# Kernel tuning notes

Measured on AMD Instinct MI355X. Metric: run time of the kernel, lower is better.

Reference implementation:

```python
import jax, jax.numpy as jnp
import numpy as np

# kernel_size=3, dilate=1 -> kernel_sample[3]=[0,1,2,3,4] selects these 5 (dy,dx) offsets
OFFSETS = [(-1, -1), (-1, 0), (-1, 1), (0, -1), (0, 0)]
EPS = 1e-12  # F.normalize default eps


def setup_inputs() -> dict:
    key = jax.random.key(0)
    x = jax.random.normal(key, (16, 192, 64, 64), dtype=jnp.float32)
    return {"x": x}


def reference(x):
    B, C, H, W = x.shape
    # ReplicationPad2d(kernel_size//2 = 1) == edge padding
    xp = jnp.pad(x, ((0, 0), (0, 0), (1, 1), (1, 1)), mode="edge")
    # centers are all interior pixels of the padded map == original pixels
    center = x.reshape(B, C, H * W).transpose(0, 2, 1)  # (B, K, C), K = H*W
    cofe = []
    for dy, dx in OFFSETS:
        side = xp[:, :, 1 + dy:1 + dy + H, 1 + dx:1 + dx + W]
        side = side.reshape(B, C, H * W).transpose(0, 2, 1)  # (B, K, C)
        # sum over K of outer products center_k (x) side_k -> (B, C, C)
        co = jnp.einsum('bkc,bkd->bcd', center, side).reshape(B, C * C)
        cofe.append(co)
    cofe = jnp.stack(cofe, axis=1)  # (B, 5, C*C)
    norm = jnp.linalg.norm(cofe, axis=-1, keepdims=True)
    return cofe / jnp.maximum(norm, EPS)
```

## Files before the change

kernel.cpp:

```cpp
#include <hip/hip_runtime.h>
#include <stdint.h>

#define C_CH 192
#define HW   4096
#define NB   16
#define NO   5

typedef __attribute__((ext_vector_type(8)))  short short8;
typedef __attribute__((ext_vector_type(16))) float floatx16;

__device__ __forceinline__ unsigned short f2bf(float f) {
    unsigned int u = __float_as_uint(f);
    unsigned int r = (u + 0x7fffu + ((u >> 16) & 1u)) >> 16;
    return (unsigned short)r;
}

__device__ __forceinline__ uint4 s8u4(short8 f) { return *(uint4*)&f; }

__device__ __forceinline__ short8 shift_m(short8 f, unsigned short ex) {
    uint4 v = *(uint4*)&f; uint4 w;
    w.x = (unsigned)ex   | (v.x << 16);
    w.y = (v.x >> 16)    | (v.y << 16);
    w.z = (v.y >> 16)    | (v.z << 16);
    w.w = (v.z >> 16)    | (v.w << 16);
    return *(short8*)&w;
}
__device__ __forceinline__ short8 shift_p(short8 f, unsigned short ex) {
    uint4 v = *(uint4*)&f; uint4 w;
    w.x = (v.x >> 16) | (v.y << 16);
    w.y = (v.y >> 16) | (v.z << 16);
    w.z = (v.z >> 16) | (v.w << 16);
    w.w = (v.w >> 16) | ((unsigned)ex << 16);
    return *(short8*)&w;
}

#define MAKE_SHIFT(Uarr, S, Um, Up)                                              \
    do {                                                                         \
        uint4 _u0 = s8u4(Uarr[(S) > 0 ? (S) - 1 : 0]);                           \
        uint4 _u1 = s8u4(Uarr[S]);                                               \
        uint4 _u2 = s8u4(Uarr[(S) < 3 ? (S) + 1 : 3]);                           \
        unsigned _sm = lo ? _u0.w : _u1.w;                                       \
        unsigned _sp = lo ? _u1.x : _u2.x;                                       \
        unsigned _rm = (unsigned)__shfl_xor((int)_sm, 32, 64);                   \
        unsigned _rp = (unsigned)__shfl_xor((int)_sp, 32, 64);                   \
        unsigned short _exm = (unsigned short)(_rm >> 16);                       \
        if ((S) == 0) _exm = lo ? _exm : (unsigned short)(_u1.x & 0xffffu);      \
        unsigned short _exp = (unsigned short)(_rp & 0xffffu);                   \
        if ((S) == 3) _exp = lo ? (unsigned short)(_u1.w >> 16) : _exp;          \
        Um = shift_m(Uarr[S], _exm);                                             \
        Up = shift_p(Uarr[S], _exp);                                             \
    } while (0)

__global__ __launch_bounds__(256) void convert_kernel(const float* __restrict__ x,
                                                      unsigned short* __restrict__ xb,
                                                      float* __restrict__ norms) {
    if (blockIdx.x == 0 && threadIdx.x < NB * NO) norms[threadIdx.x] = 0.0f;
    int t   = blockIdx.x * 256 + threadIdx.x;
    int grp = t >> 14;
    int idx = t & 16383;
    int qhi = idx >> 8;
    int cp  = (idx >> 3) & 31;
    int qlo = idx & 7;
    int q   = qhi * 8 + qlo;
    int b   = grp / 6;
    int cb  = grp - b * 6;
    int ch  = cb * 32 + cp;
    const float4* p = (const float4*)(x + (size_t)(b * C_CH + ch) * HW + q * 8);
    float4 v0 = p[0], v1 = p[1];
    ushort4 o0, o1;
    o0.x = f2bf(v0.x); o0.y = f2bf(v0.y); o0.z = f2bf(v0.z); o0.w = f2bf(v0.w);
    o1.x = f2bf(v1.x); o1.y = f2bf(v1.y); o1.z = f2bf(v1.z); o1.w = f2bf(v1.w);
    ushort4* dst = (ushort4*)xb + ((size_t)grp * 16384 + q * 32 + cp) * 2;
    dst[0] = o0; dst[1] = o1;
}

__global__ __launch_bounds__(512) void cofe_gemm(const unsigned short* __restrict__ xb,
                                                 float* __restrict__ out,
                                                 float* __restrict__ norms) {
    constexpr int RW = 8;
    int blk  = blockIdx.x;
    int work = (blk & 7) * 72 + (blk >> 3);
    int b = work / 36;
    int t = work % 36;
    int cbA = t / 6, cbB = t % 6;
    int c0 = cbA * 32, d0 = cbB * 32;

    int wv   = threadIdx.x >> 6;
    int lane = threadIdx.x & 63;
    int lr   = lane & 31;
    int lo   = lane >> 5;
    int laneoff = lo * 32 + lr;

    const short8* A8 = (const short8*)xb + (size_t)(b * 6 + cbA) * 16384;
    const short8* B8 = (const short8*)xb + (size_t)(b * 6 + cbB) * 16384;

    floatx16 acc[5];
    #pragma unroll
    for (int o = 0; o < 5; ++o)
        #pragma unroll
        for (int e = 0; e < 16; ++e)
            acc[o][e] = 0.0f;

    int h0 = wv * RW;

    short8 U[2][4];
    short8 A[3][4];

    #pragma unroll
    for (int s = 0; s < 4; ++s) {
        U[0][s] = B8[(8 * h0 + 2 * s) * 32 + laneoff];
        A[0][s] = A8[(8 * h0 + 2 * s) * 32 + laneoff];
        A[1][s] = A8[(8 * (h0 + 1) + 2 * s) * 32 + laneoff];
    }

    if (h0 == 0) {
        #pragma unroll
        for (int s = 0; s < 4; ++s) {
            short8 Um, Up;
            MAKE_SHIFT(U[0], s, Um, Up);
            acc[0] = __builtin_amdgcn_mfma_f32_32x32x16_bf16(A[0][s], Um,      acc[0], 0, 0, 0);
            acc[1] = __builtin_amdgcn_mfma_f32_32x32x16_bf16(A[0][s], U[0][s], acc[1], 0, 0, 0);
            acc[2] = __builtin_amdgcn_mfma_f32_32x32x16_bf16(A[0][s], Up,      acc[2], 0, 0, 0);
        }
    }

    #pragma unroll
    for (int r = 0; r < RW; ++r) {
        int g  = h0 + r;
        const int cu = r & 1, nx = (r + 1) & 1;
        const int ia = r % 3, ib = (r + 1) % 3, ic = (r + 2) % 3;
        int ga = (g + 2 < 64) ? g + 2 : 63;
        int gu = (g + 1 < 64) ? g + 1 : 63;
        #pragma unroll
        for (int s = 0; s < 4; ++s) {
            A[ic][s] = A8[(8 * ga + 2 * s) * 32 + laneoff];
            U[nx][s] = B8[(8 * gu + 2 * s) * 32 + laneoff];

            short8 Um, Up;
            MAKE_SHIFT(U[cu], s, Um, Up);

            acc[4] = __builtin_amdgcn_mfma_f32_32x32x16_bf16(A[ia][s], U[cu][s], acc[4], 0, 0, 0);
            acc[3] = __builtin_amdgcn_mfma_f32_32x32x16_bf16(A[ia][s], Um,       acc[3], 0, 0, 0);
            if (r + 1 < RW || g < 63) {
                acc[1] = __builtin_amdgcn_mfma_f32_32x32x16_bf16(A[ib][s], U[cu][s], acc[1], 0, 0, 0);
                acc[0] = __builtin_amdgcn_mfma_f32_32x32x16_bf16(A[ib][s], Um,       acc[0], 0, 0, 0);
                acc[2] = __builtin_amdgcn_mfma_f32_32x32x16_bf16(A[ib][s], Up,       acc[2], 0, 0, 0);
            }
        }
    }

    __shared__ float red[8192];
    __shared__ float wsum[4];
    float4* red4 = (float4*)red;
    size_t obase = (size_t)b * NO * (C_CH * C_CH);
    int tt = threadIdx.x;

    for (int o = 0; o < 5; ++o) {
        __syncthreads();
        #pragma unroll
        for (int reg = 0; reg < 16; ++reg) {
            int row = (reg & 3) + 8 * (reg >> 2) + 4 * lo;
            red[wv * 1024 + row * 32 + lr] = acc[o][reg];
        }
        __syncthreads();
        if (tt < 256) {
            float4 s = red4[tt];
            #pragma unroll
            for (int seg = 1; seg < 8; ++seg) {
                float4 v = red4[seg * 256 + tt];
                s.x += v.x; s.y += v.y; s.z += v.z; s.w += v.w;
            }
            int row = tt >> 3;
            int col = (tt & 7) * 4;
            float* op = out + obase + (size_t)o * (C_CH * C_CH)
                      + (size_t)(c0 + row) * C_CH + d0 + col;
            *(float4*)op = s;

            float ss = s.x * s.x + s.y * s.y + s.z * s.z + s.w * s.w;
            #pragma unroll
            for (int off = 32; off; off >>= 1) ss += __shfl_down(ss, off, 64);
            if (lane == 0) wsum[tt >> 6] = ss;
        }
        __syncthreads();
        if (tt == 0) atomicAdd(&norms[b * NO + o], wsum[0] + wsum[1] + wsum[2] + wsum[3]);
    }
}

__global__ __launch_bounds__(256) void scale_kernel(float* __restrict__ out,
                                                    const float* __restrict__ norms) {
    int g  = blockIdx.x * 256 + threadIdx.x;
    int bo = blockIdx.x / 36;
    float s = norms[bo];
    float inv = 1.0f / fmaxf(sqrtf(s), 1e-12f);
    float4 v = ((const float4*)out)[g];
    v.x *= inv; v.y *= inv; v.z *= inv; v.w *= inv;
    ((float4*)out)[g] = v;
}

extern "C" void kernel_launch(void* const* d_in, const int* in_sizes, int n_in,
                              void* d_out, int out_size, void* d_ws, size_t ws_size,
                              hipStream_t stream) {
    const float* x = (const float*)d_in[0];
    float* out = (float*)d_out;
    float* norms = (float*)d_ws;
    unsigned short* xb = (unsigned short*)((char*)d_ws + 512);

    convert_kernel<<<6144, 256, 0, stream>>>(x, xb, norms);
    cofe_gemm<<<576, 512, 0, stream>>>(xb, out, norms);
    scale_kernel<<<2880, 256, 0, stream>>>(out, norms);
}
```

Baseline: 130.1 us.

## Split cofe GEMM into two passes to cut accumulator registers and raise occupancy

The main GEMM loop now runs twice. The first pass accumulates only the two same-row offsets (3, 4) and reduces and stores them. The second pass reloads the inputs and accumulates the three upper-row offsets (0, 1, 2). This cuts live accumulators from five 16-float tiles to at most three and the A buffers from three sets to one, and launch bounds now request 4 waves per EU, aiming for higher occupancy. In exchange, each block reads its input tiles from global memory twice and runs the loop overhead twice.

```diff
diff --git a/kernel.cpp b/kernel.cpp
--- a/kernel.cpp
+++ b/kernel.cpp
@@ -49,6 +49,17 @@
         if ((S) == 3) _exp = lo ? (unsigned short)(_u1.w >> 16) : _exp;          \
         Um = shift_m(Uarr[S], _exm);                                             \
         Up = shift_p(Uarr[S], _exp);                                             \
+    } while (0)
+
+#define MAKE_SHIFT_M(Uarr, S, Um)                                                \
+    do {                                                                         \
+        uint4 _u0 = s8u4(Uarr[(S) > 0 ? (S) - 1 : 0]);                           \
+        uint4 _u1 = s8u4(Uarr[S]);                                               \
+        unsigned _sm = lo ? _u0.w : _u1.w;                                       \
+        unsigned _rm = (unsigned)__shfl_xor((int)_sm, 32, 64);                   \
+        unsigned short _exm = (unsigned short)(_rm >> 16);                       \
+        if ((S) == 0) _exm = lo ? _exm : (unsigned short)(_u1.x & 0xffffu);      \
+        Um = shift_m(Uarr[S], _exm);                                             \
     } while (0)
 
 __global__ __launch_bounds__(256) void convert_kernel(const float* __restrict__ x,
@@ -74,10 +85,9 @@
     dst[0] = o0; dst[1] = o1;
 }
 
-__global__ __launch_bounds__(512) void cofe_gemm(const unsigned short* __restrict__ xb,
-                                                 float* __restrict__ out,
-                                                 float* __restrict__ norms) {
-    constexpr int RW = 8;
+__global__ __launch_bounds__(512, 4) void cofe_gemm(const unsigned short* __restrict__ xb,
+                                                    float* __restrict__ out,
+                                                    float* __restrict__ norms) {
     int blk  = blockIdx.x;
     int work = (blk & 7) * 72 + (blk >> 3);
     int b = work / 36;
@@ -94,60 +104,7 @@
     const short8* A8 = (const short8*)xb + (size_t)(b * 6 + cbA) * 16384;
     const short8* B8 = (const short8*)xb + (size_t)(b * 6 + cbB) * 16384;
 
-    floatx16 acc[5];
-    #pragma unroll
-    for (int o = 0; o < 5; ++o)
-        #pragma unroll
-        for (int e = 0; e < 16; ++e)
-            acc[o][e] = 0.0f;
-
-    int h0 = wv * RW;
-
-    short8 U[2][4];
-    short8 A[3][4];
-
-    #pragma unroll
-    for (int s = 0; s < 4; ++s) {
-        U[0][s] = B8[(8 * h0 + 2 * s) * 32 + laneoff];
-        A[0][s] = A8[(8 * h0 + 2 * s) * 32 + laneoff];
-        A[1][s] = A8[(8 * (h0 + 1) + 2 * s) * 32 + laneoff];
-    }
-
-    if (h0 == 0) {
-        #pragma unroll
-        for (int s = 0; s < 4; ++s) {
-            short8 Um, Up;
-            MAKE_SHIFT(U[0], s, Um, Up);
-            acc[0] = __builtin_amdgcn_mfma_f32_32x32x16_bf16(A[0][s], Um,      acc[0], 0, 0, 0);
-            acc[1] = __builtin_amdgcn_mfma_f32_32x32x16_bf16(A[0][s], U[0][s], acc[1], 0, 0, 0);
-            acc[2] = __builtin_amdgcn_mfma_f32_32x32x16_bf16(A[0][s], Up,      acc[2], 0, 0, 0);
-        }
-    }
-
-    #pragma unroll
-    for (int r = 0; r < RW; ++r) {
-        int g  = h0 + r;
-        const int cu = r & 1, nx = (r + 1) & 1;
-        const int ia = r % 3, ib = (r + 1) % 3, ic = (r + 2) % 3;
-        int ga = (g + 2 < 64) ? g + 2 : 63;
-        int gu = (g + 1 < 64) ? g + 1 : 63;
-        #pragma unroll
-        for (int s = 0; s < 4; ++s) {
-            A[ic][s] = A8[(8 * ga + 2 * s) * 32 + laneoff];
-            U[nx][s] = B8[(8 * gu + 2 * s) * 32 + laneoff];
-
-            short8 Um, Up;
-            MAKE_SHIFT(U[cu], s, Um, Up);
-
-            acc[4] = __builtin_amdgcn_mfma_f32_32x32x16_bf16(A[ia][s], U[cu][s], acc[4], 0, 0, 0);
-            acc[3] = __builtin_amdgcn_mfma_f32_32x32x16_bf16(A[ia][s], Um,       acc[3], 0, 0, 0);
-            if (r + 1 < RW || g < 63) {
-                acc[1] = __builtin_amdgcn_mfma_f32_32x32x16_bf16(A[ib][s], U[cu][s], acc[1], 0, 0, 0);
-                acc[0] = __builtin_amdgcn_mfma_f32_32x32x16_bf16(A[ib][s], Um,       acc[0], 0, 0, 0);
-                acc[2] = __builtin_amdgcn_mfma_f32_32x32x16_bf16(A[ib][s], Up,       acc[2], 0, 0, 0);
-            }
-        }
-    }
+    int h0 = wv * 8;
 
     __shared__ float red[8192];
     __shared__ float wsum[4];
@@ -155,35 +112,119 @@
     size_t obase = (size_t)b * NO * (C_CH * C_CH);
     int tt = threadIdx.x;
 
-    for (int o = 0; o < 5; ++o) {
-        __syncthreads();
-        #pragma unroll
-        for (int reg = 0; reg < 16; ++reg) {
-            int row = (reg & 3) + 8 * (reg >> 2) + 4 * lo;
-            red[wv * 1024 + row * 32 + lr] = acc[o][reg];
-        }
-        __syncthreads();
-        if (tt < 256) {
-            float4 s = red4[tt];
+#define REDUCE_STORE(ACC, O)                                                     \
+    do {                                                                         \
+        __syncthreads();                                                         \
+        _Pragma("unroll")                                                        \
+        for (int reg = 0; reg < 16; ++reg) {                                     \
+            int row_ = (reg & 3) + 8 * (reg >> 2) + 4 * lo;      \
+            red[wv * 1024 + row_ * 32 + lr] = ACC[reg];                          \
+        }                                                                        \
+        __syncthreads();                                                         \
+        if (tt < 256) {                                                          \
+            float4 sv = red4[tt];                                                \
+            _Pragma("unroll")                                                    \
+            for (int seg = 1; seg < 8; ++seg) {                                  \
+                float4 v = red4[seg * 256 + tt];                                 \
+                sv.x += v.x; sv.y += v.y; sv.z += v.z; sv.w += v.w;              \
+            }                                                                    \
+            int row_ = tt >> 3;                                                  \
+            int col_ = (tt & 7) * 4;                                             \
+            float* op = out + obase + (size_t)(O) * (C_CH * C_CH)                \
+                      + (size_t)(c0 + row_) * C_CH + d0 + col_;                  \
+            *(float4*)op = sv;                                                   \
+            float ss = sv.x * sv.x + sv.y * sv.y + sv.z * sv.z + sv.w * sv.w;    \
+            _Pragma("unroll")                                                    \
+            for (int off = 32; off; off >>= 1) ss += __shfl_down(ss, off, 64);   \
+            if (lane == 0) wsum[tt >> 6] = ss;                                   \
+        }                                                                        \
+        __syncthreads();                                                         \
+        if (tt == 0) atomicAdd(&norms[b * NO + (O)],                             \
+                               wsum[0] + wsum[1] + wsum[2] + wsum[3]);           \
+    } while (0)
+
+    short8 A[4];
+    short8 U[2][4];
+
+    {
+        floatx16 acc3, acc4;
+        #pragma unroll
+        for (int e = 0; e < 16; ++e) { acc3[e] = 0.0f; acc4[e] = 0.0f; }
+
+        #pragma unroll
+        for (int s = 0; s < 4; ++s) {
+            A[s]    = A8[(8 * h0 + 2 * s) * 32 + laneoff];
+            U[0][s] = B8[(8 * h0 + 2 * s) * 32 + laneoff];
+        }
+
+        #pragma unroll
+        for (int r = 0; r < 8; ++r) {
+            int g = h0 + r;
+            const int cu = r & 1, nx = (r + 1) & 1;
+            int gn = (g + 1 < 64) ? g + 1 : 63;
             #pragma unroll
-            for (int seg = 1; seg < 8; ++seg) {
-                float4 v = red4[seg * 256 + tt];
-                s.x += v.x; s.y += v.y; s.z += v.z; s.w += v.w;
+            for (int s = 0; s < 4; ++s) {
+                short8 Um;
+                MAKE_SHIFT_M(U[cu], s, Um);
+                acc4 = __builtin_amdgcn_mfma_f32_32x32x16_bf16(A[s], U[cu][s], acc4, 0, 0, 0);
+                acc3 = __builtin_amdgcn_mfma_f32_32x32x16_bf16(A[s], Um,       acc3, 0, 0, 0);
+                A[s]     = A8[(8 * gn + 2 * s) * 32 + laneoff];
+                U[nx][s] = B8[(8 * gn + 2 * s) * 32 + laneoff];
             }
-            int row = tt >> 3;
-            int col = (tt & 7) * 4;
-            float* op = out + obase + (size_t)o * (C_CH * C_CH)
-                      + (size_t)(c0 + row) * C_CH + d0 + col;
-            *(float4*)op = s;
-
-            float ss = s.x * s.x + s.y * s.y + s.z * s.z + s.w * s.w;
+        }
+
+        REDUCE_STORE(acc3, 3);
+        REDUCE_STORE(acc4, 4);
+    }
+
+    {
+        floatx16 acc0, acc1, acc2;
+        #pragma unroll
+        for (int e = 0; e < 16; ++e) { acc0[e] = 0.0f; acc1[e] = 0.0f; acc2[e] = 0.0f; }
+
+        #pragma unroll
+        for (int s = 0; s < 4; ++s) {
+            A[s]    = A8[(8 * (h0 + 1) + 2 * s) * 32 + laneoff];
+            U[0][s] = B8[(8 * h0 + 2 * s) * 32 + laneoff];
+        }
+
+        if (h0 == 0) {
             #pragma unroll
-            for (int off = 32; off; off >>= 1) ss += __shfl_down(ss, off, 64);
-            if (lane == 0) wsum[tt >> 6] = ss;
-        }
-        __syncthreads();
-        if (tt == 0) atomicAdd(&norms[b * NO + o], wsum[0] + wsum[1] + wsum[2] + wsum[3]);
+            for (int s = 0; s < 4; ++s) {
+                short8 A0 = A8[(2 * s) * 32 + laneoff];
+                short8 Um, Up;
+                MAKE_SHIFT(U[0], s, Um, Up);
+                acc0 = __builtin_amdgcn_mfma_f32_32x32x16_bf16(A0, Um,      acc0, 0, 0, 0);
+                acc1 = __builtin_amdgcn_mfma_f32_32x32x16_bf16(A0, U[0][s], acc1, 0, 0, 0);
+                acc2 = __builtin_amdgcn_mfma_f32_32x32x16_bf16(A0, Up,      acc2, 0, 0, 0);
+            }
+        }
+
+        #pragma unroll
+        for (int r = 0; r < 8; ++r) {
+            int g = h0 + r;
+            const int cu = r & 1, nx = (r + 1) & 1;
+            int gn  = (g + 1 < 64) ? g + 1 : 63;
+            int gnA = (g + 2 < 64) ? g + 2 : 63;
+            #pragma unroll
+            for (int s = 0; s < 4; ++s) {
+                if (r < 7 || g < 63) {
+                    short8 Um, Up;
+                    MAKE_SHIFT(U[cu], s, Um, Up);
+                    acc1 = __builtin_amdgcn_mfma_f32_32x32x16_bf16(A[s], U[cu][s], acc1, 0, 0, 0);
+                    acc0 = __builtin_amdgcn_mfma_f32_32x32x16_bf16(A[s], Um,       acc0, 0, 0, 0);
+                    acc2 = __builtin_amdgcn_mfma_f32_32x32x16_bf16(A[s], Up,       acc2, 0, 0, 0);
+                }
+                A[s]     = A8[(8 * gnA + 2 * s) * 32 + laneoff];
+                U[nx][s] = B8[(8 * gn  + 2 * s) * 32 + laneoff];
+            }
+        }
+
+        REDUCE_STORE(acc0, 0);
+        REDUCE_STORE(acc1, 1);
+        REDUCE_STORE(acc2, 2);
     }
+#undef REDUCE_STORE
 }
 
 __global__ __launch_bounds__(256) void scale_kernel(float* __restrict__ out,
```

New measurement: 139.0 us. 1.07x slower.

## Compute two A channel blocks per workgroup with fewer waves and longer row strips

Applied to the files above, without the earlier changes.

Each workgroup now computes a 64x32 output tile (two 32-row A blocks) sharing one B/shift stream, so each loaded B fragment and its shifted variants feed twice as many MFMAs. Waves per block drop from 8 to 4, each covering 16 rows instead of 8, and the grid halves to 288 blocks, which reduces the cross-wave shared-memory reduction work. The cost is doubled accumulator registers (10 floatx16), forcing one block per CU, fewer blocks than CUs, and lower latency hiding.

```diff
diff --git a/kernel.cpp b/kernel.cpp
--- a/kernel.cpp
+++ b/kernel.cpp
@@ -74,16 +74,16 @@
     dst[0] = o0; dst[1] = o1;
 }
 
-__global__ __launch_bounds__(512) void cofe_gemm(const unsigned short* __restrict__ xb,
-                                                 float* __restrict__ out,
-                                                 float* __restrict__ norms) {
-    constexpr int RW = 8;
+__global__ __launch_bounds__(256, 1) void cofe_gemm(const unsigned short* __restrict__ xb,
+                                                    float* __restrict__ out,
+                                                    float* __restrict__ norms) {
+    constexpr int RW = 16;
     int blk  = blockIdx.x;
-    int work = (blk & 7) * 72 + (blk >> 3);
-    int b = work / 36;
-    int t = work % 36;
-    int cbA = t / 6, cbB = t % 6;
-    int c0 = cbA * 32, d0 = cbB * 32;
+    int work = (blk & 7) * 36 + (blk >> 3);
+    int b = work / 18;
+    int t = work % 18;
+    int cbA2 = t / 6, cbB = t % 6;
+    int d0 = cbB * 32;
 
     int wv   = threadIdx.x >> 6;
     int lane = threadIdx.x & 63;
@@ -91,26 +91,29 @@
     int lo   = lane >> 5;
     int laneoff = lo * 32 + lr;
 
-    const short8* A8 = (const short8*)xb + (size_t)(b * 6 + cbA) * 16384;
-    const short8* B8 = (const short8*)xb + (size_t)(b * 6 + cbB) * 16384;
-
-    floatx16 acc[5];
+    const short8* A8a = (const short8*)xb + (size_t)(b * 6 + cbA2 * 2) * 16384;
+    const short8* A8b = A8a + 16384;
+    const short8* B8  = (const short8*)xb + (size_t)(b * 6 + cbB) * 16384;
+
+    floatx16 acc_a[5], acc_b[5];
     #pragma unroll
     for (int o = 0; o < 5; ++o)
         #pragma unroll
-        for (int e = 0; e < 16; ++e)
-            acc[o][e] = 0.0f;
+        for (int e = 0; e < 16; ++e) { acc_a[o][e] = 0.0f; acc_b[o][e] = 0.0f; }
 
     int h0 = wv * RW;
 
     short8 U[2][4];
-    short8 A[3][4];
+    short8 Aa[3][4];
+    short8 Ab[3][4];
 
     #pragma unroll
     for (int s = 0; s < 4; ++s) {
-        U[0][s] = B8[(8 * h0 + 2 * s) * 32 + laneoff];
-        A[0][s] = A8[(8 * h0 + 2 * s) * 32 + laneoff];
-        A[1][s] = A8[(8 * (h0 + 1) + 2 * s) * 32 + laneoff];
+        U[0][s]  = B8 [(8 * h0 + 2 * s) * 32 + laneoff];
+        Aa[0][s] = A8a[(8 * h0 + 2 * s) * 32 + laneoff];
+        Ab[0][s] = A8b[(8 * h0 + 2 * s) * 32 + laneoff];
+        Aa[1][s] = A8a[(8 * (h0 + 1) + 2 * s) * 32 + laneoff];
+        Ab[1][s] = A8b[(8 * (h0 + 1) + 2 * s) * 32 + laneoff];
     }
 
     if (h0 == 0) {
@@ -118,9 +121,12 @@
         for (int s = 0; s < 4; ++s) {
             short8 Um, Up;
             MAKE_SHIFT(U[0], s, Um, Up);
-            acc[0] = __builtin_amdgcn_mfma_f32_32x32x16_bf16(A[0][s], Um,      acc[0], 0, 0, 0);
-            acc[1] = __builtin_amdgcn_mfma_f32_32x32x16_bf16(A[0][s], U[0][s], acc[1], 0, 0, 0);
-            acc[2] = __builtin_amdgcn_mfma_f32_32x32x16_bf16(A[0][s], Up,      acc[2], 0, 0, 0);
+            acc_a[0] = __builtin_amdgcn_mfma_f32_32x32x16_bf16(Aa[0][s], Um,      acc_a[0], 0, 0, 0);
+            acc_a[1] = __builtin_amdgcn_mfma_f32_32x32x16_bf16(Aa[0][s], U[0][s], acc_a[1], 0, 0, 0);
+            acc_a[2] = __builtin_amdgcn_mfma_f32_32x32x16_bf16(Aa[0][s], Up,      acc_a[2], 0, 0, 0);
+            acc_b[0] = __builtin_amdgcn_mfma_f32_32x32x16_bf16(Ab[0][s], Um,      acc_b[0], 0, 0, 0);
+            acc_b[1] = __builtin_amdgcn_mfma_f32_32x32x16_bf16(Ab[0][s], U[0][s], acc_b[1], 0, 0, 0);
+            acc_b[2] = __builtin_amdgcn_mfma_f32_32x32x16_bf16(Ab[0][s], Up,      acc_b[2], 0, 0, 0);
         }
     }
 
@@ -133,57 +139,66 @@
         int gu = (g + 1 < 64) ? g + 1 : 63;
         #pragma unroll
         for (int s = 0; s < 4; ++s) {
-            A[ic][s] = A8[(8 * ga + 2 * s) * 32 + laneoff];
-            U[nx][s] = B8[(8 * gu + 2 * s) * 32 + laneoff];
+            Aa[ic][s] = A8a[(8 * ga + 2 * s) * 32 + laneoff];
+            Ab[ic][s] = A8b[(8 * ga + 2 * s) * 32 + laneoff];
+            U[nx][s]  = B8 [(8 * gu + 2 * s) * 32 + laneoff];
 
             short8 Um, Up;
             MAKE_SHIFT(U[cu], s, Um, Up);
 
-            acc[4] = __builtin_amdgcn_mfma_f32_32x32x16_bf16(A[ia][s], U[cu][s], acc[4], 0, 0, 0);
-            acc[3] = __builtin_amdgcn_mfma_f32_32x32x16_bf16(A[ia][s], Um,       acc[3], 0, 0, 0);
+            acc_a[4] = __builtin_amdgcn_mfma_f32_32x32x16_bf16(Aa[ia][s], U[cu][s], acc_a[4], 0, 0, 0);
+            acc_b[4] = __builtin_amdgcn_mfma_f32_32x32x16_bf16(Ab[ia][s], U[cu][s], acc_b[4], 0, 0, 0);
+            acc_a[3] = __builtin_amdgcn_mfma_f32_32x32x16_bf16(Aa[ia][s], Um,       acc_a[3], 0, 0, 0);
+            acc_b[3] = __builtin_amdgcn_mfma_f32_32x32x16_bf16(Ab[ia][s], Um,       acc_b[3], 0, 0, 0);
             if (r + 1 < RW || g < 63) {
-                acc[1] = __builtin_amdgcn_mfma_f32_32x32x16_bf16(A[ib][s], U[cu][s], acc[1], 0, 0, 0);
-                acc[0] = __builtin_amdgcn_mfma_f32_32x32x16_bf16(A[ib][s], Um,       acc[0], 0, 0, 0);
-                acc[2] = __builtin_amdgcn_mfma_f32_32x32x16_bf16(A[ib][s], Up,       acc[2], 0, 0, 0);
+                acc_a[1] = __builtin_amdgcn_mfma_f32_32x32x16_bf16(Aa[ib][s], U[cu][s], acc_a[1], 0, 0, 0);
+                acc_b[1] = __builtin_amdgcn_mfma_f32_32x32x16_bf16(Ab[ib][s], U[cu][s], acc_b[1], 0, 0, 0);
+                acc_a[0] = __builtin_amdgcn_mfma_f32_32x32x16_bf16(Aa[ib][s], Um,       acc_a[0], 0, 0, 0);
+                acc_b[0] = __builtin_amdgcn_mfma_f32_32x32x16_bf16(Ab[ib][s], Um,       acc_b[0], 0, 0, 0);
+                acc_a[2] = __builtin_amdgcn_mfma_f32_32x32x16_bf16(Aa[ib][s], Up,       acc_a[2], 0, 0, 0);
+                acc_b[2] = __builtin_amdgcn_mfma_f32_32x32x16_bf16(Ab[ib][s], Up,       acc_b[2], 0, 0, 0);
             }
         }
     }
 
-    __shared__ float red[8192];
+    __shared__ float red[4096];
     __shared__ float wsum[4];
     float4* red4 = (float4*)red;
     size_t obase = (size_t)b * NO * (C_CH * C_CH);
     int tt = threadIdx.x;
 
-    for (int o = 0; o < 5; ++o) {
-        __syncthreads();
-        #pragma unroll
-        for (int reg = 0; reg < 16; ++reg) {
-            int row = (reg & 3) + 8 * (reg >> 2) + 4 * lo;
-            red[wv * 1024 + row * 32 + lr] = acc[o][reg];
-        }
-        __syncthreads();
-        if (tt < 256) {
-            float4 s = red4[tt];
-            #pragma unroll
-            for (int seg = 1; seg < 8; ++seg) {
-                float4 v = red4[seg * 256 + tt];
-                s.x += v.x; s.y += v.y; s.z += v.z; s.w += v.w;
-            }
-            int row = tt >> 3;
-            int col = (tt & 7) * 4;
-            float* op = out + obase + (size_t)o * (C_CH * C_CH)
-                      + (size_t)(c0 + row) * C_CH + d0 + col;
-            *(float4*)op = s;
-
-            float ss = s.x * s.x + s.y * s.y + s.z * s.z + s.w * s.w;
-            #pragma unroll
-            for (int off = 32; off; off >>= 1) ss += __shfl_down(ss, off, 64);
-            if (lane == 0) wsum[tt >> 6] = ss;
-        }
-        __syncthreads();
-        if (tt == 0) atomicAdd(&norms[b * NO + o], wsum[0] + wsum[1] + wsum[2] + wsum[3]);
-    }
+#define EPILOGUE(ACC, C0)                                                        \
+    for (int o = 0; o < 5; ++o) {                                                \
+        __syncthreads();                                                         \
+        _Pragma("unroll")                                                        \
+        for (int reg = 0; reg < 16; ++reg) {                                     \
+            int row_ = (reg & 3) + 8 * (reg >> 2) + 4 * lo;      \
+            red[wv * 1024 + row_ * 32 + lr] = ACC[o][reg];                       \
+        }                                                                        \
+        __syncthreads();                                                         \
+        float4 sv = red4[tt];                                                    \
+        _Pragma("unroll")                                                        \
+        for (int seg = 1; seg < 4; ++seg) {                                      \
+            float4 v = red4[seg * 256 + tt];                                     \
+            sv.x += v.x; sv.y += v.y; sv.z += v.z; sv.w += v.w;                  \
+        }                                                                        \
+        int row_ = tt >> 3;                                                      \
+        int col_ = (tt & 7) * 4;                                                 \
+        float* op = out + obase + (size_t)o * (C_CH * C_CH)                      \
+                  + (size_t)((C0) + row_) * C_CH + d0 + col_;                    \
+        *(float4*)op = sv;                                                       \
+        float ss = sv.x * sv.x + sv.y * sv.y + sv.z * sv.z + sv.w * sv.w;        \
+        _Pragma("unroll")                                                        \
+        for (int off = 32; off; off >>= 1) ss += __shfl_down(ss, off, 64);       \
+        if (lane == 0) wsum[wv] = ss;                                            \
+        __syncthreads();                                                         \
+        if (tt == 0) atomicAdd(&norms[b * NO + o],                               \
+                               wsum[0] + wsum[1] + wsum[2] + wsum[3]);           \
+    }
+
+    EPILOGUE(acc_a, cbA2 * 64)
+    EPILOGUE(acc_b, cbA2 * 64 + 32)
+#undef EPILOGUE
 }
 
 __global__ __launch_bounds__(256) void scale_kernel(float* __restrict__ out,
@@ -206,6 +221,6 @@
     unsigned short* xb = (unsigned short*)((char*)d_ws + 512);
 
     convert_kernel<<<6144, 256, 0, stream>>>(x, xb, norms);
-    cofe_gemm<<<576, 512, 0, stream>>>(xb, out, norms);
+    cofe_gemm<<<288, 256, 0, stream>>>(xb, out, norms);
     scale_kernel<<<2880, 256, 0, stream>>>(out, norms);
 }
```

After: 151.1 us. 1.16x slower.

## Precompute shifted bf16 panels in convert kernel and halve GEMM block width

Applied to the files above, without the earlier changes.

The convert kernel now writes three bf16 panels: the center and copies shifted one pixel left and right, with edge replication handled through wave shuffles. The GEMM kernel then loads these shifted operands directly instead of building them with per-iteration shuffles and bit shifts. The GEMM also drops from 8 to 4 waves per block, each covering 16 rows instead of 8, so the cross-wave LDS reduction is shorter, and launch bounds request 2 blocks per CU. The cost is three times the workspace writes and triple B-operand global traffic, plus more register pressure and less row parallelism per block.

```diff
diff --git a/kernel.cpp b/kernel.cpp
--- a/kernel.cpp
+++ b/kernel.cpp
@@ -5,6 +5,7 @@
 #define HW   4096
 #define NB   16
 #define NO   5
+#define PANEL 25165824
 
 typedef __attribute__((ext_vector_type(8)))  short short8;
 typedef __attribute__((ext_vector_type(16))) float floatx16;
@@ -15,44 +16,10 @@
     return (unsigned short)r;
 }
 
-__device__ __forceinline__ uint4 s8u4(short8 f) { return *(uint4*)&f; }
-
-__device__ __forceinline__ short8 shift_m(short8 f, unsigned short ex) {
-    uint4 v = *(uint4*)&f; uint4 w;
-    w.x = (unsigned)ex   | (v.x << 16);
-    w.y = (v.x >> 16)    | (v.y << 16);
-    w.z = (v.y >> 16)    | (v.z << 16);
-    w.w = (v.z >> 16)    | (v.w << 16);
-    return *(short8*)&w;
-}
-__device__ __forceinline__ short8 shift_p(short8 f, unsigned short ex) {
-    uint4 v = *(uint4*)&f; uint4 w;
-    w.x = (v.x >> 16) | (v.y << 16);
-    w.y = (v.y >> 16) | (v.z << 16);
-    w.z = (v.z >> 16) | (v.w << 16);
-    w.w = (v.w >> 16) | ((unsigned)ex << 16);
-    return *(short8*)&w;
-}
-
-#define MAKE_SHIFT(Uarr, S, Um, Up)                                              \
-    do {                                                                         \
-        uint4 _u0 = s8u4(Uarr[(S) > 0 ? (S) - 1 : 0]);                           \
-        uint4 _u1 = s8u4(Uarr[S]);                                               \
-        uint4 _u2 = s8u4(Uarr[(S) < 3 ? (S) + 1 : 3]);                           \
-        unsigned _sm = lo ? _u0.w : _u1.w;                                       \
-        unsigned _sp = lo ? _u1.x : _u2.x;                                       \
-        unsigned _rm = (unsigned)__shfl_xor((int)_sm, 32, 64);                   \
-        unsigned _rp = (unsigned)__shfl_xor((int)_sp, 32, 64);                   \
-        unsigned short _exm = (unsigned short)(_rm >> 16);                       \
-        if ((S) == 0) _exm = lo ? _exm : (unsigned short)(_u1.x & 0xffffu);      \
-        unsigned short _exp = (unsigned short)(_rp & 0xffffu);                   \
-        if ((S) == 3) _exp = lo ? (unsigned short)(_u1.w >> 16) : _exp;          \
-        Um = shift_m(Uarr[S], _exm);                                             \
-        Up = shift_p(Uarr[S], _exp);                                             \
-    } while (0)
-
 __global__ __launch_bounds__(256) void convert_kernel(const float* __restrict__ x,
                                                       unsigned short* __restrict__ xb,
+                                                      unsigned short* __restrict__ xbm,
+                                                      unsigned short* __restrict__ xbp,
                                                       float* __restrict__ norms) {
     if (blockIdx.x == 0 && threadIdx.x < NB * NO) norms[threadIdx.x] = 0.0f;
     int t   = blockIdx.x * 256 + threadIdx.x;
@@ -67,17 +34,41 @@
     int ch  = cb * 32 + cp;
     const float4* p = (const float4*)(x + (size_t)(b * C_CH + ch) * HW + q * 8);
     float4 v0 = p[0], v1 = p[1];
-    ushort4 o0, o1;
-    o0.x = f2bf(v0.x); o0.y = f2bf(v0.y); o0.z = f2bf(v0.z); o0.w = f2bf(v0.w);
-    o1.x = f2bf(v1.x); o1.y = f2bf(v1.y); o1.z = f2bf(v1.z); o1.w = f2bf(v1.w);
-    ushort4* dst = (ushort4*)xb + ((size_t)grp * 16384 + q * 32 + cp) * 2;
-    dst[0] = o0; dst[1] = o1;
-}
-
-__global__ __launch_bounds__(512) void cofe_gemm(const unsigned short* __restrict__ xb,
-                                                 float* __restrict__ out,
-                                                 float* __restrict__ norms) {
-    constexpr int RW = 8;
+    unsigned u0 = (unsigned)f2bf(v0.x) | ((unsigned)f2bf(v0.y) << 16);
+    unsigned u1 = (unsigned)f2bf(v0.z) | ((unsigned)f2bf(v0.w) << 16);
+    unsigned u2 = (unsigned)f2bf(v1.x) | ((unsigned)f2bf(v1.y) << 16);
+    unsigned u3 = (unsigned)f2bf(v1.z) | ((unsigned)f2bf(v1.w) << 16);
+
+    unsigned prev_u3 = (unsigned)__shfl_up((int)u3, 1, 64);
+    unsigned next_u0 = (unsigned)__shfl_down((int)u0, 1, 64);
+    unsigned short exm = (qlo == 0) ? (unsigned short)(u0 & 0xffffu)
+                                    : (unsigned short)(prev_u3 >> 16);
+    unsigned short exp_ = (qlo == 7) ? (unsigned short)(u3 >> 16)
+                                     : (unsigned short)(next_u0 & 0xffffu);
+
+    uint4 cen = {u0, u1, u2, u3};
+    uint4 um, up;
+    um.x = (unsigned)exm | (u0 << 16);
+    um.y = (u0 >> 16)    | (u1 << 16);
+    um.z = (u1 >> 16)    | (u2 << 16);
+    um.w = (u2 >> 16)    | (u3 << 16);
+    up.x = (u0 >> 16)    | (u1 << 16);
+    up.y = (u1 >> 16)    | (u2 << 16);
+    up.z = (u2 >> 16)    | (u3 << 16);
+    up.w = (u3 >> 16)    | ((unsigned)exp_ << 16);
+
+    size_t oct = (size_t)grp * 16384 + q * 32 + cp;
+    ((uint4*)xb)[oct]  = cen;
+    ((uint4*)xbm)[oct] = um;
+    ((uint4*)xbp)[oct] = up;
+}
+
+__global__ __launch_bounds__(256, 2) void cofe_gemm(const unsigned short* __restrict__ xb,
+                                                    const unsigned short* __restrict__ xbm,
+                                                    const unsigned short* __restrict__ xbp,
+                                                    float* __restrict__ out,
+                                                    float* __restrict__ norms) {
+    constexpr int RW = 16;
     int blk  = blockIdx.x;
     int work = (blk & 7) * 72 + (blk >> 3);
     int b = work / 36;
@@ -91,8 +82,10 @@
     int lo   = lane >> 5;
     int laneoff = lo * 32 + lr;
 
-    const short8* A8 = (const short8*)xb + (size_t)(b * 6 + cbA) * 16384;
-    const short8* B8 = (const short8*)xb + (size_t)(b * 6 + cbB) * 16384;
+    const short8* A8  = (const short8*)xb  + (size_t)(b * 6 + cbA) * 16384;
+    const short8* U8  = (const short8*)xb  + (size_t)(b * 6 + cbB) * 16384;
+    const short8* Um8 = (const short8*)xbm + (size_t)(b * 6 + cbB) * 16384;
+    const short8* Up8 = (const short8*)xbp + (size_t)(b * 6 + cbB) * 16384;
 
     floatx16 acc[5];
     #pragma unroll
@@ -103,24 +96,24 @@
 
     int h0 = wv * RW;
 
-    short8 U[2][4];
     short8 A[3][4];
+    short8 U[2][4], Um[2][4], Up[2][4];
 
     #pragma unroll
     for (int s = 0; s < 4; ++s) {
-        U[0][s] = B8[(8 * h0 + 2 * s) * 32 + laneoff];
-        A[0][s] = A8[(8 * h0 + 2 * s) * 32 + laneoff];
-        A[1][s] = A8[(8 * (h0 + 1) + 2 * s) * 32 + laneoff];
+        U[0][s]  = U8 [(8 * h0 + 2 * s) * 32 + laneoff];
+        Um[0][s] = Um8[(8 * h0 + 2 * s) * 32 + laneoff];
+        Up[0][s] = Up8[(8 * h0 + 2 * s) * 32 + laneoff];
+        A[0][s]  = A8 [(8 * h0 + 2 * s) * 32 + laneoff];
+        A[1][s]  = A8 [(8 * (h0 + 1) + 2 * s) * 32 + laneoff];
     }
 
     if (h0 == 0) {
         #pragma unroll
         for (int s = 0; s < 4; ++s) {
-            short8 Um, Up;
-            MAKE_SHIFT(U[0], s, Um, Up);
-            acc[0] = __builtin_amdgcn_mfma_f32_32x32x16_bf16(A[0][s], Um,      acc[0], 0, 0, 0);
-            acc[1] = __builtin_amdgcn_mfma_f32_32x32x16_bf16(A[0][s], U[0][s], acc[1], 0, 0, 0);
-            acc[2] = __builtin_amdgcn_mfma_f32_32x32x16_bf16(A[0][s], Up,      acc[2], 0, 0, 0);
+            acc[0] = __builtin_amdgcn_mfma_f32_32x32x16_bf16(A[0][s], Um[0][s], acc[0], 0, 0, 0);
+            acc[1] = __builtin_amdgcn_mfma_f32_32x32x16_bf16(A[0][s], U[0][s],  acc[1], 0, 0, 0);
+            acc[2] = __builtin_amdgcn_mfma_f32_32x32x16_bf16(A[0][s], Up[0][s], acc[2], 0, 0, 0);
         }
     }
 
@@ -133,23 +126,22 @@
         int gu = (g + 1 < 64) ? g + 1 : 63;
         #pragma unroll
         for (int s = 0; s < 4; ++s) {
-            A[ic][s] = A8[(8 * ga + 2 * s) * 32 + laneoff];
-            U[nx][s] = B8[(8 * gu + 2 * s) * 32 + laneoff];
-
-            short8 Um, Up;
-            MAKE_SHIFT(U[cu], s, Um, Up);
-
-            acc[4] = __builtin_amdgcn_mfma_f32_32x32x16_bf16(A[ia][s], U[cu][s], acc[4], 0, 0, 0);
-            acc[3] = __builtin_amdgcn_mfma_f32_32x32x16_bf16(A[ia][s], Um,       acc[3], 0, 0, 0);
+            A[ic][s]  = A8 [(8 * ga + 2 * s) * 32 + laneoff];
+            U[nx][s]  = U8 [(8 * gu + 2 * s) * 32 + laneoff];
+            Um[nx][s] = Um8[(8 * gu + 2 * s) * 32 + laneoff];
+            Up[nx][s] = Up8[(8 * gu + 2 * s) * 32 + laneoff];
+
+            acc[4] = __builtin_amdgcn_mfma_f32_32x32x16_bf16(A[ia][s], U[cu][s],  acc[4], 0, 0, 0);
+            acc[3] = __builtin_amdgcn_mfma_f32_32x32x16_bf16(A[ia][s], Um[cu][s], acc[3], 0, 0, 0);
             if (r + 1 < RW || g < 63) {
-                acc[1] = __builtin_amdgcn_mfma_f32_32x32x16_bf16(A[ib][s], U[cu][s], acc[1], 0, 0, 0);
-                acc[0] = __builtin_amdgcn_mfma_f32_32x32x16_bf16(A[ib][s], Um,       acc[0], 0, 0, 0);
-                acc[2] = __builtin_amdgcn_mfma_f32_32x32x16_bf16(A[ib][s], Up,       acc[2], 0, 0, 0);
+                acc[1] = __builtin_amdgcn_mfma_f32_32x32x16_bf16(A[ib][s], U[cu][s],  acc[1], 0, 0, 0);
+                acc[0] = __builtin_amdgcn_mfma_f32_32x32x16_bf16(A[ib][s], Um[cu][s], acc[0], 0, 0, 0);
+                acc[2] = __builtin_amdgcn_mfma_f32_32x32x16_bf16(A[ib][s], Up[cu][s], acc[2], 0, 0, 0);
             }
         }
     }
 
-    __shared__ float red[8192];
+    __shared__ float red[4096];
     __shared__ float wsum[4];
     float4* red4 = (float4*)red;
     size_t obase = (size_t)b * NO * (C_CH * C_CH);
@@ -163,26 +155,25 @@
             red[wv * 1024 + row * 32 + lr] = acc[o][reg];
         }
         __syncthreads();
-        if (tt < 256) {
-            float4 s = red4[tt];
-            #pragma unroll
-            for (int seg = 1; seg < 8; ++seg) {
-                float4 v = red4[seg * 256 + tt];
-                s.x += v.x; s.y += v.y; s.z += v.z; s.w += v.w;
-            }
-            int row = tt >> 3;
-            int col = (tt & 7) * 4;
-            float* op = out + obase + (size_t)o * (C_CH * C_CH)
-                      + (size_t)(c0 + row) * C_CH + d0 + col;
-            *(float4*)op = s;
-
-            float ss = s.x * s.x + s.y * s.y + s.z * s.z + s.w * s.w;
-            #pragma unroll
-            for (int off = 32; off; off >>= 1) ss += __shfl_down(ss, off, 64);
-            if (lane == 0) wsum[tt >> 6] = ss;
-        }
+        float4 sv = red4[tt];
+        #pragma unroll
+        for (int seg = 1; seg < 4; ++seg) {
+            float4 v = red4[seg * 256 + tt];
+            sv.x += v.x; sv.y += v.y; sv.z += v.z; sv.w += v.w;
+        }
+        int row = tt >> 3;
+        int col = (tt & 7) * 4;
+        float* op = out + obase + (size_t)o * (C_CH * C_CH)
+                  + (size_t)(c0 + row) * C_CH + d0 + col;
+        *(float4*)op = sv;
+
+        float ss = sv.x * sv.x + sv.y * sv.y + sv.z * sv.z + sv.w * sv.w;
+        #pragma unroll
+        for (int off = 32; off; off >>= 1) ss += __shfl_down(ss, off, 64);
+        if (lane == 0) wsum[wv] = ss;
         __syncthreads();
-        if (tt == 0) atomicAdd(&norms[b * NO + o], wsum[0] + wsum[1] + wsum[2] + wsum[3]);
+        if (tt == 0) atomicAdd(&norms[b * NO + o],
+                               wsum[0] + wsum[1] + wsum[2] + wsum[3]);
     }
 }
 
@@ -203,9 +194,11 @@
     const float* x = (const float*)d_in[0];
     float* out = (float*)d_out;
     float* norms = (float*)d_ws;
-    unsigned short* xb = (unsigned short*)((char*)d_ws + 512);
-
-    convert_kernel<<<6144, 256, 0, stream>>>(x, xb, norms);
-    cofe_gemm<<<576, 512, 0, stream>>>(xb, out, norms);
+    unsigned short* xb  = (unsigned short*)((char*)d_ws + 512);
+    unsigned short* xbm = (unsigned short*)((char*)d_ws + 512 + (size_t)PANEL);
+    unsigned short* xbp = (unsigned short*)((char*)d_ws + 512 + 2 * (size_t)PANEL);
+
+    convert_kernel<<<6144, 256, 0, stream>>>(x, xb, xbm, xbp, norms);
+    cofe_gemm<<<576, 256, 0, stream>>>(xb, xbm, xbp, out, norms);
     scale_kernel<<<2880, 256, 0, stream>>>(out, norms);
 }
```

New measurement: 149.0 us. +14.5%, slower.
